# Kernel optimization log

Measured on AMD Instinct MI355X. Metric: run time of the kernel, lower is better.

The kernel has to match this reference:

```python
import jax, jax.numpy as jnp
import numpy as np

EPS = 1e-12  # torch F.normalize eps

def _l2_normalize(x):
    n = jnp.linalg.norm(x, axis=-1, keepdims=True)
    return x / jnp.maximum(n, EPS)

def setup_inputs() -> dict:
    key = jax.random.key(0)
    k1, k2 = jax.random.split(key)
    B, F = 8192, 128
    z1 = jax.random.normal(k1, (B, F), dtype=jnp.float32)
    z2 = jax.random.normal(k2, (B, F), dtype=jnp.float32)
    return {"z1": z1, "z2": z2}

def reference(z1, z2):
    T = 1.0
    z1n = _l2_normalize(z1)
    z2n = _l2_normalize(z2)
    # Full similarity matrix S[i,j] = <z1n_i, z2n_j>.
    # Original builds logits row i = [S_ii, S_ij (j != i)], which is a
    # permutation of row i of S; CE with label 0 = logsumexp(row) - S_ii.
    S = jnp.einsum('bf,cf->bc', z1n, z2n) / T  # [B, B]
    pos = jnp.diagonal(S)                       # [B]
    lse = jax.nn.logsumexp(S, axis=1)           # [B]
    return jnp.mean(lse - pos)
```

## Files before the change

### kernel.cpp

```cpp
#include <hip/hip_runtime.h>
#include <hip/hip_bf16.h>

typedef __attribute__((ext_vector_type(8))) short bf16x8;
typedef __attribute__((ext_vector_type(4))) float f32x4;

#define B_ROWS 8192
#define FDIM 128
#define NT_TILES 16
#define NCHUNK 16

#define GLOAD_LDS(gp, lp) __builtin_amdgcn_global_load_lds( \
    (const __attribute__((address_space(1))) unsigned*)(gp), \
    (__attribute__((address_space(3))) unsigned*)(lp), 16, 0, 0)

#define LOG2E 1.4426950408889634f

__global__ __launch_bounds__(256) void simclr_norm(const float* __restrict__ z1,
                                                   const float* __restrict__ z2,
                                                   __hip_bfloat16* __restrict__ z1n,
                                                   __hip_bfloat16* __restrict__ z2n,
                                                   float* __restrict__ pos) {
    int row  = (blockIdx.x * 256 + threadIdx.x) >> 6;
    int lane = threadIdx.x & 63;
    int c = lane * 2;
    const float2 v1 = *(const float2*)(z1 + row * FDIM + c);
    const float2 v2 = *(const float2*)(z2 + row * FDIM + c);
    float s1 = v1.x * v1.x + v1.y * v1.y;
    float s2 = v2.x * v2.x + v2.y * v2.y;
    for (int m = 32; m > 0; m >>= 1) { s1 += __shfl_xor(s1, m); s2 += __shfl_xor(s2, m); }
    float inv1 = 1.0f / fmaxf(sqrtf(s1), 1e-12f);
    float inv2 = 1.0f / fmaxf(sqrtf(s2), 1e-12f);
    float a0 = v1.x * inv1, a1 = v1.y * inv1;
    float b0 = v2.x * inv2, b1 = v2.y * inv2;
    z1n[row * FDIM + c]     = __float2bfloat16(a0 * LOG2E);
    z1n[row * FDIM + c + 1] = __float2bfloat16(a1 * LOG2E);
    z2n[row * FDIM + c]     = __float2bfloat16(b0);
    z2n[row * FDIM + c + 1] = __float2bfloat16(b1);
    float p = a0 * b0 + a1 * b1;
    for (int m = 32; m > 0; m >>= 1) p += __shfl_xor(p, m);
    if (lane == 0) pos[row] = p;
}

__global__ __launch_bounds__(256) void simclr_gemm(const __hip_bfloat16* __restrict__ z1n,
                                                   const __hip_bfloat16* __restrict__ z2n,
                                                   float* __restrict__ rsPart) {
    __shared__ unsigned char smem[65536];
    const int tid = threadIdx.x;
    const int wid = tid >> 6, lane = tid & 63;
    const int lq = lane >> 4, lr = lane & 15;
    const int rowBase = blockIdx.y * 256 + wid * 64;
    const int colBase = blockIdx.x * (NT_TILES * 32);
    unsigned char* myLds = smem + wid * 16384;

    const unsigned short* g1 = (const unsigned short*)z1n;
    const unsigned short* g2 = (const unsigned short*)z2n;

    const unsigned short* bsrc0 = g2 + (size_t)(colBase + lq) * FDIM + (lr ^ lq) * 8;
    const unsigned short* bsrc1 = g2 + (size_t)(colBase + lq) * FDIM + (lr ^ (4 + lq)) * 8;

#define STAGE(t, buf) do {                                                        \
        _Pragma("unroll")                                                         \
        for (int j = 0; j < 8; ++j) {                                             \
            const unsigned short* gp = ((j & 1) ? bsrc1 : bsrc0)                  \
                                       + (size_t)((t) * 32 + j * 4) * FDIM;       \
            GLOAD_LDS(gp, myLds + (buf) * 8192 + j * 1024);                       \
        }                                                                         \
    } while (0)

    STAGE(0, 0);

    bf16x8 a[4][4];
#pragma unroll
    for (int m = 0; m < 4; ++m) {
        const unsigned short* rp = g1 + (size_t)(rowBase + m * 16 + lr) * FDIM + lq * 8;
#pragma unroll
        for (int kk = 0; kk < 4; ++kk)
            a[m][kk] = *(const bf16x8*)(rp + kk * 32);
    }

    float rowsum[4][4] = {};
    const f32x4 z4 = {0.0f, 0.0f, 0.0f, 0.0f};

    for (int t = 0; t < NT_TILES; ++t) {
        const int cur = t & 1;
        if (t + 1 < NT_TILES) {
            STAGE(t + 1, cur ^ 1);
            asm volatile("s_waitcnt vmcnt(8)" ::: "memory");
        } else {
            asm volatile("s_waitcnt vmcnt(0)" ::: "memory");
        }

        const unsigned char* bp = myLds + cur * 8192;
        f32x4 acc[4][2];
        {
            bf16x8 b0 = *(const bf16x8*)(bp + lr * 256 + ((lq * 16) ^ ((lr & 7) << 4)));
            bf16x8 b1 = *(const bf16x8*)(bp + (16 + lr) * 256 + ((lq * 16) ^ ((lr & 7) << 4)));
#pragma unroll
            for (int m = 0; m < 4; ++m) {
                acc[m][0] = __builtin_amdgcn_mfma_f32_16x16x32_bf16(a[m][0], b0, z4, 0, 0, 0);
                acc[m][1] = __builtin_amdgcn_mfma_f32_16x16x32_bf16(a[m][0], b1, z4, 0, 0, 0);
            }
        }
#pragma unroll
        for (int kk = 1; kk < 4; ++kk) {
            bf16x8 b0 = *(const bf16x8*)(bp + lr * 256 + ((kk * 64 + lq * 16) ^ ((lr & 7) << 4)));
            bf16x8 b1 = *(const bf16x8*)(bp + (16 + lr) * 256 + ((kk * 64 + lq * 16) ^ ((lr & 7) << 4)));
#pragma unroll
            for (int m = 0; m < 4; ++m) {
                acc[m][0] = __builtin_amdgcn_mfma_f32_16x16x32_bf16(a[m][kk], b0, acc[m][0], 0, 0, 0);
                acc[m][1] = __builtin_amdgcn_mfma_f32_16x16x32_bf16(a[m][kk], b1, acc[m][1], 0, 0, 0);
            }
        }
#pragma unroll
        for (int m = 0; m < 4; ++m)
#pragma unroll
            for (int r = 0; r < 4; ++r)
                rowsum[m][r] += exp2f(acc[m][0][r]) + exp2f(acc[m][1][r]);
    }
#undef STAGE

#pragma unroll
    for (int m = 0; m < 4; ++m)
#pragma unroll
        for (int r = 0; r < 4; ++r) {
            float s = rowsum[m][r];
            s += __shfl_xor(s, 1); s += __shfl_xor(s, 2);
            s += __shfl_xor(s, 4); s += __shfl_xor(s, 8);
            if (lr == 0)
                rsPart[blockIdx.x * B_ROWS + rowBase + m * 16 + lq * 4 + r] = s;
        }
}

__global__ __launch_bounds__(256) void simclr_finish(const float* __restrict__ rsPart,
                                                     const float* __restrict__ pos,
                                                     float* __restrict__ out) {
    __shared__ float red[4];
    int i = blockIdx.x * 256 + threadIdx.x;
    float R = 0.0f;
#pragma unroll
    for (int c = 0; c < NCHUNK; ++c) R += rsPart[c * B_ROWS + i];
    float s = logf(R) - pos[i];
    for (int m = 32; m > 0; m >>= 1) s += __shfl_xor(s, m);
    if ((threadIdx.x & 63) == 0) red[threadIdx.x >> 6] = s;
    __syncthreads();
    if (threadIdx.x == 0) {
        float v = (red[0] + red[1]) + (red[2] + red[3]);
        atomicAdd(out, v * (1.0f / (float)B_ROWS));
    }
}

extern "C" void kernel_launch(void* const* d_in, const int* in_sizes, int n_in,
                              void* d_out, int out_size, void* d_ws, size_t ws_size,
                              hipStream_t stream) {
    const float* z1 = (const float*)d_in[0];
    const float* z2 = (const float*)d_in[1];
    float* out = (float*)d_out;
    char* ws = (char*)d_ws;

    __hip_bfloat16* z1n = (__hip_bfloat16*)ws;
    __hip_bfloat16* z2n = (__hip_bfloat16*)(ws + 2097152);
    float* pos          = (float*)(ws + 4194304);
    float* rsPart       = (float*)(ws + 4194304 + 32768);

    hipMemsetAsync(out, 0, sizeof(float), stream);
    simclr_norm<<<B_ROWS / 4, 256, 0, stream>>>(z1, z2, z1n, z2n, pos);
    simclr_gemm<<<dim3(NCHUNK, 32), 256, 0, stream>>>(z1n, z2n, rsPart);
    simclr_finish<<<B_ROWS / 256, 256, 0, stream>>>(rsPart, pos, out);
}
```

Measured before the change: 49.78 us.

## Retile GEMM so waves share rows, split columns, and use fast exp2

The four waves of a block now share the same 64 rows and each takes its own 256-column chunk, instead of each owning different rows over a 512-column span. Column tiles shrink to 16 with a manually unrolled double buffer, and the LDS per block halves. The grid grows to 1024 blocks and 32 column chunks, and the finish kernel's NCHUNK reduction loop now sums 32 partials. Other changes: MFMA chains are interleaved across m with s_setprio around them, LDS addresses are precomputed, and exp2f is replaced by the raw v_exp_f32 instruction. The aim is higher occupancy and parallelism, with more partial writes and smaller tiles as the cost.

```diff
diff --git a/kernel.cpp b/kernel.cpp
--- a/kernel.cpp
+++ b/kernel.cpp
@@ -6,14 +6,24 @@
 
 #define B_ROWS 8192
 #define FDIM 128
-#define NT_TILES 16
-#define NCHUNK 16
+#define WAVE_COLS 256
+#define TILE_COLS 16
+#define NT 16
+#define NCHUNK 32
 
 #define GLOAD_LDS(gp, lp) __builtin_amdgcn_global_load_lds( \
     (const __attribute__((address_space(1))) unsigned*)(gp), \
     (__attribute__((address_space(3))) unsigned*)(lp), 16, 0, 0)
 
 #define LOG2E 1.4426950408889634f
+
+#if __has_builtin(__builtin_amdgcn_exp2f)
+__device__ __forceinline__ float fast_exp2(float x) { return __builtin_amdgcn_exp2f(x); }
+#else
+__device__ __forceinline__ float fast_exp2(float x) {
+    float r; asm("v_exp_f32 %0, %1\n\ts_nop 0" : "=v"(r) : "v"(x)); return r;
+}
+#endif
 
 __global__ __launch_bounds__(256) void simclr_norm(const float* __restrict__ z1,
                                                    const float* __restrict__ z2,
@@ -44,13 +54,14 @@
 __global__ __launch_bounds__(256) void simclr_gemm(const __hip_bfloat16* __restrict__ z1n,
                                                    const __hip_bfloat16* __restrict__ z2n,
                                                    float* __restrict__ rsPart) {
-    __shared__ unsigned char smem[65536];
+    __shared__ unsigned char smem[32768];
     const int tid = threadIdx.x;
     const int wid = tid >> 6, lane = tid & 63;
     const int lq = lane >> 4, lr = lane & 15;
-    const int rowBase = blockIdx.y * 256 + wid * 64;
-    const int colBase = blockIdx.x * (NT_TILES * 32);
-    unsigned char* myLds = smem + wid * 16384;
+    const int rowBase = blockIdx.y * 64;
+    const int chunk = blockIdx.x * 4 + wid;
+    const int colBase = chunk * WAVE_COLS;
+    unsigned char* myLds = smem + wid * 8192;
 
     const unsigned short* g1 = (const unsigned short*)z1n;
     const unsigned short* g2 = (const unsigned short*)z2n;
@@ -60,12 +71,15 @@
 
 #define STAGE(t, buf) do {                                                        \
         _Pragma("unroll")                                                         \
-        for (int j = 0; j < 8; ++j) {                                             \
+        for (int j = 0; j < 4; ++j) {                                             \
             const unsigned short* gp = ((j & 1) ? bsrc1 : bsrc0)                  \
-                                       + (size_t)((t) * 32 + j * 4) * FDIM;       \
-            GLOAD_LDS(gp, myLds + (buf) * 8192 + j * 1024);                       \
+                                       + (size_t)((t) * TILE_COLS + j * 4) * FDIM;\
+            GLOAD_LDS(gp, myLds + (buf) + j * 1024);                              \
         }                                                                         \
     } while (0)
+
+#define VMCNT4 asm volatile("s_waitcnt vmcnt(4)" ::: "memory")
+#define VMCNT0 asm volatile("s_waitcnt vmcnt(0)" ::: "memory")
 
     STAGE(0, 0);
 
@@ -78,46 +92,57 @@
             a[m][kk] = *(const bf16x8*)(rp + kk * 32);
     }
 
+    int rdA[4];
+#pragma unroll
+    for (int kk = 0; kk < 4; ++kk)
+        rdA[kk] = lr * 256 + ((kk * 64 + lq * 16) ^ ((lr & 7) << 4));
+
     float rowsum[4][4] = {};
     const f32x4 z4 = {0.0f, 0.0f, 0.0f, 0.0f};
 
-    for (int t = 0; t < NT_TILES; ++t) {
-        const int cur = t & 1;
-        if (t + 1 < NT_TILES) {
-            STAGE(t + 1, cur ^ 1);
-            asm volatile("s_waitcnt vmcnt(8)" ::: "memory");
-        } else {
-            asm volatile("s_waitcnt vmcnt(0)" ::: "memory");
-        }
+#define COMPUTE(buf) do {                                                         \
+        const unsigned char* bp = myLds + (buf);                                  \
+        bf16x8 b0 = *(const bf16x8*)(bp + rdA[0]);                                \
+        bf16x8 b1 = *(const bf16x8*)(bp + rdA[1]);                                \
+        bf16x8 b2 = *(const bf16x8*)(bp + rdA[2]);                                \
+        bf16x8 b3 = *(const bf16x8*)(bp + rdA[3]);                                \
+        f32x4 acc[4];                                                             \
+        __builtin_amdgcn_s_setprio(1);                                            \
+        _Pragma("unroll")                                                         \
+        for (int m = 0; m < 4; ++m)                                               \
+            acc[m] = __builtin_amdgcn_mfma_f32_16x16x32_bf16(a[m][0], b0, z4, 0, 0, 0); \
+        _Pragma("unroll")                                                         \
+        for (int m = 0; m < 4; ++m)                                               \
+            acc[m] = __builtin_amdgcn_mfma_f32_16x16x32_bf16(a[m][1], b1, acc[m], 0, 0, 0); \
+        _Pragma("unroll")                                                         \
+        for (int m = 0; m < 4; ++m)                                               \
+            acc[m] = __builtin_amdgcn_mfma_f32_16x16x32_bf16(a[m][2], b2, acc[m], 0, 0, 0); \
+        _Pragma("unroll")                                                         \
+        for (int m = 0; m < 4; ++m)                                               \
+            acc[m] = __builtin_amdgcn_mfma_f32_16x16x32_bf16(a[m][3], b3, acc[m], 0, 0, 0); \
+        __builtin_amdgcn_s_setprio(0);                                            \
+        _Pragma("unroll")                                                         \
+        for (int m = 0; m < 4; ++m)                                               \
+            _Pragma("unroll")                                                     \
+            for (int r = 0; r < 4; ++r)                                           \
+                rowsum[m][r] += fast_exp2(acc[m][r]);                             \
+    } while (0)
 
-        const unsigned char* bp = myLds + cur * 8192;
-        f32x4 acc[4][2];
-        {
-            bf16x8 b0 = *(const bf16x8*)(bp + lr * 256 + ((lq * 16) ^ ((lr & 7) << 4)));
-            bf16x8 b1 = *(const bf16x8*)(bp + (16 + lr) * 256 + ((lq * 16) ^ ((lr & 7) << 4)));
-#pragma unroll
-            for (int m = 0; m < 4; ++m) {
-                acc[m][0] = __builtin_amdgcn_mfma_f32_16x16x32_bf16(a[m][0], b0, z4, 0, 0, 0);
-                acc[m][1] = __builtin_amdgcn_mfma_f32_16x16x32_bf16(a[m][0], b1, z4, 0, 0, 0);
-            }
-        }
-#pragma unroll
-        for (int kk = 1; kk < 4; ++kk) {
-            bf16x8 b0 = *(const bf16x8*)(bp + lr * 256 + ((kk * 64 + lq * 16) ^ ((lr & 7) << 4)));
-            bf16x8 b1 = *(const bf16x8*)(bp + (16 + lr) * 256 + ((kk * 64 + lq * 16) ^ ((lr & 7) << 4)));
-#pragma unroll
-            for (int m = 0; m < 4; ++m) {
-                acc[m][0] = __builtin_amdgcn_mfma_f32_16x16x32_bf16(a[m][kk], b0, acc[m][0], 0, 0, 0);
-                acc[m][1] = __builtin_amdgcn_mfma_f32_16x16x32_bf16(a[m][kk], b1, acc[m][1], 0, 0, 0);
-            }
-        }
-#pragma unroll
-        for (int m = 0; m < 4; ++m)
-#pragma unroll
-            for (int r = 0; r < 4; ++r)
-                rowsum[m][r] += exp2f(acc[m][0][r]) + exp2f(acc[m][1][r]);
+    for (int tp = 0; tp < 7; ++tp) {
+        STAGE(2 * tp + 1, 4096);
+        VMCNT4;
+        COMPUTE(0);
+        STAGE(2 * tp + 2, 0);
+        VMCNT4;
+        COMPUTE(4096);
     }
+    STAGE(15, 4096);
+    VMCNT4;
+    COMPUTE(0);
+    VMCNT0;
+    COMPUTE(4096);
 #undef STAGE
+#undef COMPUTE
 
 #pragma unroll
     for (int m = 0; m < 4; ++m)
@@ -127,7 +152,7 @@
             s += __shfl_xor(s, 1); s += __shfl_xor(s, 2);
             s += __shfl_xor(s, 4); s += __shfl_xor(s, 8);
             if (lr == 0)
-                rsPart[blockIdx.x * B_ROWS + rowBase + m * 16 + lq * 4 + r] = s;
+                rsPart[chunk * B_ROWS + rowBase + m * 16 + lq * 4 + r] = s;
         }
 }
 
@@ -164,6 +189,6 @@
 
     hipMemsetAsync(out, 0, sizeof(float), stream);
     simclr_norm<<<B_ROWS / 4, 256, 0, stream>>>(z1, z2, z1n, z2n, pos);
-    simclr_gemm<<<dim3(NCHUNK, 32), 256, 0, stream>>>(z1n, z2n, rsPart);
+    simclr_gemm<<<dim3(8, 128), 256, 0, stream>>>(z1n, z2n, rsPart);
     simclr_finish<<<B_ROWS / 256, 256, 0, stream>>>(rsPart, pos, out);
 }
```

Measured after the change: 57.85 us. 16.2% more time.

## Switch similarity GEMM to FP8 scaled MFMA with per-wave column chunks

Applied to the files above, without the earlier changes.

Normalized embeddings are quantized to FP8 e4m3 instead of bf16, and the GEMM uses the 16x16x128 f8f6f4 scaled MFMA so each tile needs a single K step. The grid is reorganized so each wave streams its own 256-column chunk with a smaller LDS footprint, and the partial-sum count doubles. The output memset is folded into the norm kernel and a hardware exp2 is used. This halves the bytes moved and the MFMA issue count, at the cost of lower precision in the logits.

```diff
diff --git a/kernel.cpp b/kernel.cpp
--- a/kernel.cpp
+++ b/kernel.cpp
@@ -1,25 +1,47 @@
 #include <hip/hip_runtime.h>
 #include <hip/hip_bf16.h>
+#include <hip/hip_fp8.h>
 
-typedef __attribute__((ext_vector_type(8))) short bf16x8;
+typedef __attribute__((ext_vector_type(8))) int i32x8;
 typedef __attribute__((ext_vector_type(4))) float f32x4;
 
 #define B_ROWS 8192
 #define FDIM 128
-#define NT_TILES 16
-#define NCHUNK 16
+#define WAVE_COLS 256
+#define NT 16
+#define NCHUNK 32
+#define LOG2E 1.4426950408889634f
 
 #define GLOAD_LDS(gp, lp) __builtin_amdgcn_global_load_lds( \
     (const __attribute__((address_space(1))) unsigned*)(gp), \
     (__attribute__((address_space(3))) unsigned*)(lp), 16, 0, 0)
 
-#define LOG2E 1.4426950408889634f
+#if __has_builtin(__builtin_amdgcn_exp2f)
+__device__ __forceinline__ float fast_exp2(float x) { return __builtin_amdgcn_exp2f(x); }
+#else
+__device__ __forceinline__ float fast_exp2(float x) {
+    float r; asm("v_exp_f32 %0, %1\n\ts_nop 0" : "=v"(r) : "v"(x)); return r;
+}
+#endif
+
+__device__ __forceinline__ unsigned short pk_fp8(float x0, float x1) {
+#if __has_builtin(__builtin_amdgcn_cvt_pk_fp8_f32)
+    return (unsigned short)(__builtin_amdgcn_cvt_pk_fp8_f32(x0, x1, 0, false) & 0xFFFF);
+#else
+    __hip_fp8_e4m3 q0(x0), q1(x1);
+    unsigned char b0, b1;
+    __builtin_memcpy(&b0, &q0, 1); __builtin_memcpy(&b1, &q1, 1);
+    return (unsigned short)(b0 | (b1 << 8));
+#endif
+}
 
 __global__ __launch_bounds__(256) void simclr_norm(const float* __restrict__ z1,
                                                    const float* __restrict__ z2,
-                                                   __hip_bfloat16* __restrict__ z1n,
-                                                   __hip_bfloat16* __restrict__ z2n,
-                                                   float* __restrict__ pos) {
+                                                   unsigned char* __restrict__ z1q,
+                                                   unsigned char* __restrict__ z2q,
+                                                   float* __restrict__ pos,
+                                                   float* __restrict__ out) {
+    if (blockIdx.x == 0 && threadIdx.x == 0) *out = 0.0f;
     int row  = (blockIdx.x * 256 + threadIdx.x) >> 6;
     int lane = threadIdx.x & 63;
     int c = lane * 2;
@@ -32,90 +54,75 @@
     float inv2 = 1.0f / fmaxf(sqrtf(s2), 1e-12f);
     float a0 = v1.x * inv1, a1 = v1.y * inv1;
     float b0 = v2.x * inv2, b1 = v2.y * inv2;
-    z1n[row * FDIM + c]     = __float2bfloat16(a0 * LOG2E);
-    z1n[row * FDIM + c + 1] = __float2bfloat16(a1 * LOG2E);
-    z2n[row * FDIM + c]     = __float2bfloat16(b0);
-    z2n[row * FDIM + c + 1] = __float2bfloat16(b1);
+    *(unsigned short*)(z1q + (size_t)row * FDIM + c) = pk_fp8(a0 * LOG2E, a1 * LOG2E);
+    *(unsigned short*)(z2q + (size_t)row * FDIM + c) = pk_fp8(b0, b1);
     float p = a0 * b0 + a1 * b1;
     for (int m = 32; m > 0; m >>= 1) p += __shfl_xor(p, m);
     if (lane == 0) pos[row] = p;
 }
 
-__global__ __launch_bounds__(256) void simclr_gemm(const __hip_bfloat16* __restrict__ z1n,
-                                                   const __hip_bfloat16* __restrict__ z2n,
+__global__ __launch_bounds__(256) void simclr_gemm(const unsigned char* __restrict__ z1q,
+                                                   const unsigned char* __restrict__ z2q,
                                                    float* __restrict__ rsPart) {
-    __shared__ unsigned char smem[65536];
+    __shared__ unsigned char smem[16384];
     const int tid = threadIdx.x;
     const int wid = tid >> 6, lane = tid & 63;
     const int lq = lane >> 4, lr = lane & 15;
-    const int rowBase = blockIdx.y * 256 + wid * 64;
-    const int colBase = blockIdx.x * (NT_TILES * 32);
-    unsigned char* myLds = smem + wid * 16384;
+    const int rowBase = blockIdx.y * 64;
+    const int chunk = blockIdx.x * 4 + wid;
+    const int colBase = chunk * WAVE_COLS;
+    unsigned char* myLds = smem + wid * 4096;
 
-    const unsigned short* g1 = (const unsigned short*)z1n;
-    const unsigned short* g2 = (const unsigned short*)z2n;
+    const int srow = lane >> 3;
+    const int sslot = (lane & 7) ^ srow;
+    const unsigned char* gsrc = z2q + (size_t)(colBase + srow) * FDIM + sslot * 16;
 
-    const unsigned short* bsrc0 = g2 + (size_t)(colBase + lq) * FDIM + (lr ^ lq) * 8;
-    const unsigned short* bsrc1 = g2 + (size_t)(colBase + lq) * FDIM + (lr ^ (4 + lq)) * 8;
-
-#define STAGE(t, buf) do {                                                        \
-        _Pragma("unroll")                                                         \
-        for (int j = 0; j < 8; ++j) {                                             \
-            const unsigned short* gp = ((j & 1) ? bsrc1 : bsrc0)                  \
-                                       + (size_t)((t) * 32 + j * 4) * FDIM;       \
-            GLOAD_LDS(gp, myLds + (buf) * 8192 + j * 1024);                       \
-        }                                                                         \
+#define STAGE(t, buf) do {                                        \
+        GLOAD_LDS(gsrc + (t) * 2048,        myLds + (buf));       \
+        GLOAD_LDS(gsrc + (t) * 2048 + 1024, myLds + (buf) + 1024);\
     } while (0)
 
     STAGE(0, 0);
 
-    bf16x8 a[4][4];
+    i32x8 a[4];
 #pragma unroll
-    for (int m = 0; m < 4; ++m) {
-        const unsigned short* rp = g1 + (size_t)(rowBase + m * 16 + lr) * FDIM + lq * 8;
-#pragma unroll
-        for (int kk = 0; kk < 4; ++kk)
-            a[m][kk] = *(const bf16x8*)(rp + kk * 32);
-    }
+    for (int m = 0; m < 4; ++m)
+        a[m] = *(const i32x8*)(z1q + (size_t)(rowBase + m * 16 + lr) * FDIM + lq * 32);
+
+    const int sw = lr << 4;
+    const int rd0 = lr * 128 + (( lq * 32      ) ^ ((lr & 7) << 4));
+    const int rd1 = lr * 128 + (((lq * 32) + 16) ^ ((lr & 7) << 4));
+    (void)sw;
 
     float rowsum[4][4] = {};
     const f32x4 z4 = {0.0f, 0.0f, 0.0f, 0.0f};
 
-    for (int t = 0; t < NT_TILES; ++t) {
-        const int cur = t & 1;
-        if (t + 1 < NT_TILES) {
-            STAGE(t + 1, cur ^ 1);
-            asm volatile("s_waitcnt vmcnt(8)" ::: "memory");
+#pragma unroll
+    for (int t = 0; t < NT; ++t) {
+        const int cur = (t & 1) * 2048;
+        if (t + 1 < NT) {
+            STAGE(t + 1, cur ^ 2048);
+            asm volatile("s_waitcnt vmcnt(2)" ::: "memory");
         } else {
             asm volatile("s_waitcnt vmcnt(0)" ::: "memory");
         }
-
-        const unsigned char* bp = myLds + cur * 8192;
-        f32x4 acc[4][2];
-        {
-            bf16x8 b0 = *(const bf16x8*)(bp + lr * 256 + ((lq * 16) ^ ((lr & 7) << 4)));
-            bf16x8 b1 = *(const bf16x8*)(bp + (16 + lr) * 256 + ((lq * 16) ^ ((lr & 7) << 4)));
+        const unsigned char* bp = myLds + cur;
+        uint4 u0 = *(const uint4*)(bp + rd0);
+        uint4 u1 = *(const uint4*)(bp + rd1);
+        i32x8 b;
+        b[0] = (int)u0.x; b[1] = (int)u0.y; b[2] = (int)u0.z; b[3] = (int)u0.w;
+        b[4] = (int)u1.x; b[5] = (int)u1.y; b[6] = (int)u1.z; b[7] = (int)u1.w;
+        f32x4 acc[4];
 #pragma unroll
-            for (int m = 0; m < 4; ++m) {
-                acc[m][0] = __builtin_amdgcn_mfma_f32_16x16x32_bf16(a[m][0], b0, z4, 0, 0, 0);
-                acc[m][1] = __builtin_amdgcn_mfma_f32_16x16x32_bf16(a[m][0], b1, z4, 0, 0, 0);
-            }
-        }
-#pragma unroll
-        for (int kk = 1; kk < 4; ++kk) {
-            bf16x8 b0 = *(const bf16x8*)(bp + lr * 256 + ((kk * 64 + lq * 16) ^ ((lr & 7) << 4)));
-            bf16x8 b1 = *(const bf16x8*)(bp + (16 + lr) * 256 + ((kk * 64 + lq * 16) ^ ((lr & 7) << 4)));
-#pragma unroll
-            for (int m = 0; m < 4; ++m) {
-                acc[m][0] = __builtin_amdgcn_mfma_f32_16x16x32_bf16(a[m][kk], b0, acc[m][0], 0, 0, 0);
-                acc[m][1] = __builtin_amdgcn_mfma_f32_16x16x32_bf16(a[m][kk], b1, acc[m][1], 0, 0, 0);
-            }
-        }
+        for (int m = 0; m < 4; ++m)
+            acc[m] = __builtin_amdgcn_mfma_scale_f32_16x16x128_f8f6f4(
+                         a[m], b, z4, 0, 0,
+                         0, 0x7F7F7F7F, 0, 0x7F7F7F7F);
 #pragma unroll
         for (int m = 0; m < 4; ++m)
 #pragma unroll
             for (int r = 0; r < 4; ++r)
-                rowsum[m][r] += exp2f(acc[m][0][r]) + exp2f(acc[m][1][r]);
+                rowsum[m][r] += fast_exp2(acc[m][r]);
     }
 #undef STAGE
 
@@ -127,7 +134,7 @@
             s += __shfl_xor(s, 1); s += __shfl_xor(s, 2);
             s += __shfl_xor(s, 4); s += __shfl_xor(s, 8);
             if (lr == 0)
-                rsPart[blockIdx.x * B_ROWS + rowBase + m * 16 + lq * 4 + r] = s;
+                rsPart[chunk * B_ROWS + rowBase + m * 16 + lq * 4 + r] = s;
         }
 }
 
@@ -157,13 +164,12 @@
     float* out = (float*)d_out;
     char* ws = (char*)d_ws;
 
-    __hip_bfloat16* z1n = (__hip_bfloat16*)ws;
-    __hip_bfloat16* z2n = (__hip_bfloat16*)(ws + 2097152);
-    float* pos          = (float*)(ws + 4194304);
-    float* rsPart       = (float*)(ws + 4194304 + 32768);
+    unsigned char* z1q = (unsigned char*)ws;
+    unsigned char* z2q = (unsigned char*)(ws + 1048576);
+    float* pos         = (float*)(ws + 2097152);
+    float* rsPart      = (float*)(ws + 2097152 + 32768);
 
-    hipMemsetAsync(out, 0, sizeof(float), stream);
-    simclr_norm<<<B_ROWS / 4, 256, 0, stream>>>(z1, z2, z1n, z2n, pos);
-    simclr_gemm<<<dim3(NCHUNK, 32), 256, 0, stream>>>(z1n, z2n, rsPart);
+    simclr_norm<<<B_ROWS / 4, 256, 0, stream>>>(z1, z2, z1q, z2q, pos, out);
+    simclr_gemm<<<dim3(8, 128), 256, 0, stream>>>(z1q, z2q, rsPart);
     simclr_finish<<<B_ROWS / 256, 256, 0, stream>>>(rsPart, pos, out);
 }
```

Result: faster. 45.92 us (-7.7%).
